# Optimization experiments

Hardware: AMD Instinct MI355X
Metric: run time of the kernel (lower is better)

## Reference

```python
import jax, jax.numpy as jnp
import numpy as np

N_SRC = 50000
N_TGT = 50000
E = 320000
D = 256          # feature dim == hidden_channels
H = 256
OUT = 16
L = 2
P_DROP = 0.1
NEG_SLOPE = 0.01  # F.leaky_relu default


def _seg_mean(x, src_idx, dst_idx, n_dst):
    # gather source features along edges, mean-aggregate per destination (PyG SAGE default aggr='mean')
    msgs = x[src_idx]                                            # [E, D]
    s = jax.ops.segment_sum(msgs, dst_idx, num_segments=n_dst)   # [n_dst, D]
    cnt = jax.ops.segment_sum(jnp.ones((dst_idx.shape[0],), x.dtype), dst_idx, num_segments=n_dst)
    return s / jnp.maximum(cnt, 1.0)[:, None]


def _dropout(x, p, key):
    keep = jax.random.bernoulli(key, 1.0 - p, x.shape)
    return jnp.where(keep, x / (1.0 - p), jnp.zeros((), x.dtype))


def setup_inputs() -> dict:
    key = jax.random.key(0)
    ks = jax.random.split(key, 16)
    sc_in = 1.0 / np.sqrt(D)
    sc_h = 1.0 / np.sqrt(H)
    inp = {
        'x_source': jax.random.normal(ks[0], (N_SRC, D), jnp.float32),
        'x_target': jax.random.normal(ks[1], (N_TGT, D), jnp.float32),
        'ei_st': jax.random.randint(ks[2], (2, E), 0, N_SRC, jnp.int32),  # row0: source idx, row1: target idx
        'ei_ts': jax.random.randint(ks[3], (2, E), 0, N_TGT, jnp.int32),  # row0: target idx, row1: source idx
        # SAGEConv params per layer per relation; lin_l has bias, lin_r does not (PyG)
        'Wl_st': jax.random.normal(ks[4], (L, D, H), jnp.float32) * sc_in,
        'Wr_st': jax.random.normal(ks[5], (L, D, H), jnp.float32) * sc_in,
        'b_st': jnp.zeros((L, H), jnp.float32),
        'Wl_ts': jax.random.normal(ks[6], (L, D, H), jnp.float32) * sc_in,
        'Wr_ts': jax.random.normal(ks[7], (L, D, H), jnp.float32) * sc_in,
        'b_ts': jnp.zeros((L, H), jnp.float32),
        'Wout': jax.random.normal(ks[8], (H, OUT), jnp.float32) * sc_h,
        'bout': jnp.zeros((OUT,), jnp.float32),
    }
    return inp


def reference(x_source, x_target, ei_st, ei_ts, Wl_st, Wr_st, b_st, Wl_ts, Wr_ts, b_ts, Wout, bout):
    drop_key = jax.random.key(42)
    x_s, x_t = x_source, x_target
    for l in range(L):
        # relation ('source','edge','target'): messages source -> target
        m_t = _seg_mean(x_s, ei_st[0], ei_st[1], N_TGT)
        new_t = m_t @ Wl_st[l] + b_st[l] + x_t @ Wr_st[l]
        # relation ('target','rev_edge','source'): messages target -> source
        m_s = _seg_mean(x_t, ei_ts[0], ei_ts[1], N_SRC)
        new_s = m_s @ Wl_ts[l] + b_ts[l] + x_s @ Wr_ts[l]
        # leaky_relu + dropout (F.dropout default training=True)
        new_s = jnp.where(new_s >= 0, new_s, NEG_SLOPE * new_s)
        new_t = jnp.where(new_t >= 0, new_t, NEG_SLOPE * new_t)
        x_s = _dropout(new_s, P_DROP, jax.random.fold_in(drop_key, 2 * l))
        x_t = _dropout(new_t, P_DROP, jax.random.fold_in(drop_key, 2 * l + 1))
    return x_s @ Wout + bout  # [N_SRC, OUT]
```

## Files before the change

### kernel.cpp

```cpp
#include <hip/hip_runtime.h>
#include <stdint.h>

#define NSRC 50000
#define NTGT 50000
#define NE   320000
#define DIN  256
#define HID  256
#define DOUT 16

#define GBM 64
#define GBLK ((NSRC + GBM - 1) / GBM)
#define MASK_DW_PER (GBLK * 512)
#define MASK_BLKS (3 * MASK_DW_PER / 256)

typedef __attribute__((ext_vector_type(8))) short bf16x8;
typedef __attribute__((ext_vector_type(4))) float f32x4;

__device__ inline ushort f2b(float f) {
  uint32_t u = __float_as_uint(f);
  return (ushort)((u + 0x7FFFu + ((u >> 16) & 1u)) >> 16);
}
__device__ inline float b2f(ushort h) { return __uint_as_float(((uint32_t)h) << 16); }

typedef __attribute__((address_space(3))) uint32_t lds_u32_t;
typedef const __attribute__((address_space(1))) uint32_t glb_u32_t;
__device__ __forceinline__ void ld_lds16(const ushort* g, ushort* lds) {
  __builtin_amdgcn_global_load_lds((glb_u32_t*)g, (lds_u32_t*)lds, 16, 0, 0);
}

__host__ __device__ constexpr uint64_t tf2x32(uint32_t k0, uint32_t k1,
                                              uint32_t x0, uint32_t x1) {
  uint32_t ks2 = k0 ^ k1 ^ 0x1BD11BDAu;
  x0 += k0; x1 += k1;
#define TF_ROT(x, r) (((x) << (r)) | ((x) >> (32 - (r))))
#define TF_RND(r) { x0 += x1; x1 = TF_ROT(x1, r) ^ x0; }
  TF_RND(13) TF_RND(15) TF_RND(26) TF_RND(6)
  x0 += k1;  x1 += ks2 + 1u;
  TF_RND(17) TF_RND(29) TF_RND(16) TF_RND(24)
  x0 += ks2; x1 += k0 + 2u;
  TF_RND(13) TF_RND(15) TF_RND(26) TF_RND(6)
  x0 += k0;  x1 += k1 + 3u;
  TF_RND(17) TF_RND(29) TF_RND(16) TF_RND(24)
  x0 += k1;  x1 += ks2 + 4u;
  TF_RND(13) TF_RND(15) TF_RND(26) TF_RND(6)
  x0 += ks2; x1 += k0 + 5u;
#undef TF_RND
#undef TF_ROT
  return (uint64_t(x0) << 32) | uint64_t(x1);
}

constexpr uint64_t FOLD[4] = {
  tf2x32(0u, 42u, 0u, 0u),
  tf2x32(0u, 42u, 0u, 1u),
  tf2x32(0u, 42u, 0u, 2u),
  tf2x32(0u, 42u, 0u, 3u),
};

__global__ __launch_bounds__(256) void cvt2_f32_bf16(const float* __restrict__ a,
                                                     const float* __restrict__ b,
                                                     ushort* __restrict__ oa,
                                                     ushort* __restrict__ ob,
                                                     int n4, int nbPer) {
  int blk = blockIdx.x;
  const float* in = blk < nbPer ? a : b;
  ushort* out = blk < nbPer ? oa : ob;
  int i = (blk % nbPer) * 256 + threadIdx.x;
  if (i >= n4) return;
  float4 v = ((const float4*)in)[i];
  ushort4 o;
  o.x = f2b(v.x); o.y = f2b(v.y); o.z = f2b(v.z); o.w = f2b(v.w);
  ((ushort4*)out)[i] = o;
}

__device__ __forceinline__ void mask_word(uint32_t* __restrict__ masks, int d) {
  int g = d / MASK_DW_PER;
  int w = d - g * MASK_DW_PER;
  int gt = w >> 1, half = w & 1;
  int gblk = gt >> 8, gtid = gt & 255;
  int wave = gtid >> 6, lane = gtid & 63;
  int q = lane >> 4, r = lane & 15;
  uint64_t fk = (g == 0) ? FOLD[1] : (g == 1 ? FOLD[0] : FOLD[2]);
  uint32_t kk0 = (uint32_t)(fk >> 32), kk1 = (uint32_t)fk;
  int mbase = gblk * GBM;
  uint32_t mword = 0;
#pragma unroll
  for (int bb = 0; bb < 32; ++bb) {
    int s = half * 32 + bb;
    int si = s >> 4, se = (s >> 2) & 3, sj = s & 3;
    uint32_t rowg = (uint32_t)(mbase + si * 16 + q * 4 + se);
    uint32_t colg = (uint32_t)(wave * 64 + sj * 16 + r);
    uint64_t rr = tf2x32(kk0, kk1, 0u, rowg * 256u + colg);
    uint32_t bits = (uint32_t)(rr >> 32) ^ (uint32_t)rr;
    mword |= (((bits >> 9) < 7549747u) ? 1u : 0u) << bb;
  }
  masks[d] = mword;
}

struct W6 {
  const float* s[6];
  ushort* d[6];
};
__global__ __launch_bounds__(256) void wcvt_t6(W6 p) {
  __shared__ ushort tile[64][65];
  int w = blockIdx.x >> 4;
  const float* W = p.s[w];
  ushort* Wt = p.d[w];
  int t = threadIdx.x;
  int ktile = (blockIdx.x >> 2) & 3, ntile = blockIdx.x & 3;
#pragma unroll
  for (int rep = 0; rep < 16; ++rep) {
    int lin = rep * 256 + t;
    int kk = lin >> 6, nn = lin & 63;
    tile[nn][kk] = f2b(W[(size_t)(ktile * 64 + kk) * 256 + ntile * 64 + nn]);
  }
  __syncthreads();
#pragma unroll
  for (int rep = 0; rep < 16; ++rep) {
    int lin = rep * 256 + t;
    int nn = lin >> 6, kk = lin & 63;
    Wt[(size_t)(ntile * 64 + nn) * 256 + ktile * 64 + kk] = tile[nn][kk];
  }
}

__global__ __launch_bounds__(256) void csr_hist2(const int* __restrict__ ei_a,
                                                 const int* __restrict__ ei_b,
                                                 int* __restrict__ cur_a,
                                                 int* __restrict__ cur_b,
                                                 int nE, int nbPer) {
  int blk = blockIdx.x;
  const int* ei = blk < nbPer ? ei_a : ei_b;
  int* cur = blk < nbPer ? cur_a : cur_b;
  int e = (blk % nbPer) * 256 + threadIdx.x;
  if (e < nE) atomicAdd(cur + ei[nE + e], 1);
}

#define SB 1024
__global__ __launch_bounds__(SB) void scan_partial(const int* __restrict__ cur_a,
                                                   const int* __restrict__ cur_b,
                                                   int* __restrict__ bsum,
                                                   int n, int nbPer) {
  __shared__ int red[SB];
  int b = blockIdx.x;
  const int* cnt = b < nbPer ? cur_a : cur_b;
  int i = (b % nbPer) * SB + threadIdx.x;
  red[threadIdx.x] = (i < n) ? cnt[i] : 0;
  __syncthreads();
  for (int d = SB / 2; d > 0; d >>= 1) {
    if (threadIdx.x < d) red[threadIdx.x] += red[threadIdx.x + d];
    __syncthreads();
  }
  if (threadIdx.x == 0) bsum[b] = red[0];
}

__global__ __launch_bounds__(128) void scan_base(int* __restrict__ bsum, int nbPer) {
  __shared__ int buf[2][64];
  int half = threadIdx.x >> 6;
  int t = threadIdx.x & 63;
  buf[half][t] = (t < nbPer) ? bsum[half * nbPer + t] : 0;
  __syncthreads();
  for (int d = 1; d < 64; d <<= 1) {
    int v = (t >= d) ? buf[half][t - d] : 0;
    __syncthreads();
    buf[half][t] += v;
    __syncthreads();
  }
  if (t < nbPer) bsum[half * nbPer + t] = (t == 0) ? 0 : buf[half][t - 1];
}

__global__ __launch_bounds__(SB) void scan_final(int* __restrict__ cur_a,
                                                 int* __restrict__ cur_b,
                                                 int* __restrict__ offs_a,
                                                 int* __restrict__ offs_b,
                                                 const int* __restrict__ bsum,
                                                 int n, int nbPer) {
  __shared__ int part[SB];
  int b = blockIdx.x;
  bool first = b < nbPer;
  int* cur = first ? cur_a : cur_b;
  int* offs = first ? offs_a : offs_b;
  int i = (b % nbPer) * SB + threadIdx.x;
  int v = (i < n) ? cur[i] : 0;
  part[threadIdx.x] = v;
  __syncthreads();
  for (int d = 1; d < SB; d <<= 1) {
    int tv = (threadIdx.x >= d) ? part[threadIdx.x - d] : 0;
    __syncthreads();
    part[threadIdx.x] += tv;
    __syncthreads();
  }
  int excl = part[threadIdx.x] - v + bsum[b];
  if (i < n) {
    offs[i] = excl;
    cur[i] = 0;
  }
  if (i == n - 1) offs[n] = excl + v;
}

__global__ __launch_bounds__(256) void csr_fill2(const int* __restrict__ ei_a,
                                                 const int* __restrict__ ei_b,
                                                 const int* __restrict__ offs_a,
                                                 const int* __restrict__ offs_b,
                                                 int* __restrict__ cur_a,
                                                 int* __restrict__ cur_b,
                                                 int* __restrict__ adj_a,
                                                 int* __restrict__ adj_b,
                                                 int nE, int nbPer) {
  int blk = blockIdx.x;
  bool first = blk < nbPer;
  const int* ei = first ? ei_a : ei_b;
  const int* offs = first ? offs_a : offs_b;
  int* cur = first ? cur_a : cur_b;
  int* adj = first ? adj_a : adj_b;
  int e = (blk % nbPer) * 256 + threadIdx.x;
  if (e >= nE) return;
  int dst = ei[nE + e];
  int pos = atomicAdd(cur + dst, 1);
  adj[offs[dst] + pos] = ei[e];
}

__device__ __forceinline__ void gather_row(const ushort* __restrict__ x,
                                           const int* __restrict__ offs,
                                           const int* __restrict__ adj,
                                           ushort* __restrict__ m,
                                           int row, int lane) {
  int start = offs[row], end = offs[row + 1];
  float a0 = 0.f, a1 = 0.f, a2 = 0.f, a3 = 0.f;
  int e = start;
  for (; e + 3 < end; e += 4) {
    int s0 = adj[e], s1 = adj[e + 1], s2 = adj[e + 2], s3 = adj[e + 3];
    ushort4 v0 = *(const ushort4*)(x + (size_t)s0 * DIN + lane * 4);
    ushort4 v1 = *(const ushort4*)(x + (size_t)s1 * DIN + lane * 4);
    ushort4 v2 = *(const ushort4*)(x + (size_t)s2 * DIN + lane * 4);
    ushort4 v3 = *(const ushort4*)(x + (size_t)s3 * DIN + lane * 4);
    a0 += b2f(v0.x); a1 += b2f(v0.y); a2 += b2f(v0.z); a3 += b2f(v0.w);
    a0 += b2f(v1.x); a1 += b2f(v1.y); a2 += b2f(v1.z); a3 += b2f(v1.w);
    a0 += b2f(v2.x); a1 += b2f(v2.y); a2 += b2f(v2.z); a3 += b2f(v2.w);
    a0 += b2f(v3.x); a1 += b2f(v3.y); a2 += b2f(v3.z); a3 += b2f(v3.w);
  }
  for (; e < end; ++e) {
    int s = adj[e];
    ushort4 v = *(const ushort4*)(x + (size_t)s * DIN + lane * 4);
    a0 += b2f(v.x); a1 += b2f(v.y); a2 += b2f(v.z); a3 += b2f(v.w);
  }
  float inv = 1.0f / fmaxf((float)(end - start), 1.0f);
  ushort4 o;
  o.x = f2b(a0 * inv); o.y = f2b(a1 * inv); o.z = f2b(a2 * inv); o.w = f2b(a3 * inv);
  *(ushort4*)(m + (size_t)row * DIN + lane * 4) = o;
}

__global__ __launch_bounds__(256) void gather_mean_h(const ushort* __restrict__ x,
                                                     const int* __restrict__ offs,
                                                     const int* __restrict__ adj,
                                                     ushort* __restrict__ m,
                                                     int nRows) {
  int row = blockIdx.x * 4 + (threadIdx.x >> 6);
  if (row >= nRows) return;
  gather_row(x, offs, adj, m, row, threadIdx.x & 63);
}

__global__ __launch_bounds__(256) void gather2m_mean_h(
    const ushort* __restrict__ xa, const int* __restrict__ offsa,
    const int* __restrict__ adja, ushort* __restrict__ ma,
    const ushort* __restrict__ xb, const int* __restrict__ offsb,
    const int* __restrict__ adjb, ushort* __restrict__ mb,
    uint32_t* __restrict__ masks, int nRows, int nbPer) {
  const int T = 2 * nbPer + MASK_BLKS;
  int blk = (int)(((long long)blockIdx.x * 97) % T);
  if (blk >= 2 * nbPer) {
    mask_word(masks, (blk - 2 * nbPer) * 256 + threadIdx.x);
    return;
  }
  bool first = blk < nbPer;
  int row = (blk % nbPer) * 4 + (threadIdx.x >> 6);
  if (row >= nRows) return;
  if (first) gather_row(xa, offsa, adja, ma, row, threadIdx.x & 63);
  else       gather_row(xb, offsb, adjb, mb, row, threadIdx.x & 63);
}

__global__ __launch_bounds__(256, 4) void gemm_dual_mfma(
    const ushort* __restrict__ A1, const ushort* __restrict__ A2,
    const ushort* __restrict__ W1t, const ushort* __restrict__ W2t,
    const float* __restrict__ bias, const uint2* __restrict__ mk,
    ushort* __restrict__ C, int M) {
  __shared__ ushort sA[2][GBM * 32];
  __shared__ ushort sB[2][HID * 32];
  const int tid = threadIdx.x;
  const int wave = tid >> 6, lane = tid & 63;
  const int q = lane >> 4, r = lane & 15;
  const int mbase = blockIdx.x * GBM;

  const uint2 km = mk[blockIdx.x * 256 + tid];

  f32x4 acc[4][4] = {};

  const int arow = tid >> 2;
  const int akc = (tid & 3) * 8;
  const int agrow = min(mbase + arow, M - 1);
  const ushort* a1p = A1 + (size_t)agrow * DIN + akc;
  const ushort* a2p = A2 + (size_t)agrow * DIN + akc;
  const ushort* w1b = W1t + (size_t)arow * DIN + akc;
  const ushort* w2b = W2t + (size_t)arow * DIN + akc;
  ushort* ldsA0 = &sA[0][wave * 512];
  ushort* ldsA1 = &sA[1][wave * 512];

#pragma unroll
  for (int t = 0; t < 8; ++t) {
    const int kt = t * 32;
    __syncthreads();
    ld_lds16(a1p + kt, ldsA0);
    ld_lds16(a2p + kt, ldsA1);
#pragma unroll
    for (int c = 0; c < 4; ++c) {
      ld_lds16(w1b + c * (64 * DIN) + kt, &sB[0][c * 2048 + wave * 512]);
      ld_lds16(w2b + c * (64 * DIN) + kt, &sB[1][c * 2048 + wave * 512]);
    }
    __syncthreads();
#pragma unroll
    for (int ph = 0; ph < 2; ++ph) {
      bf16x8 af[4], bfr[4];
#pragma unroll
      for (int i = 0; i < 4; ++i)
        af[i] = *(const bf16x8*)&sA[ph][(i * 16 + r) * 32 + q * 8];
#pragma unroll
      for (int j = 0; j < 4; ++j)
        bfr[j] = *(const bf16x8*)&sB[ph][(wave * 64 + j * 16 + r) * 32 + q * 8];
#pragma unroll
      for (int i = 0; i < 4; ++i)
#pragma unroll
        for (int j = 0; j < 4; ++j)
          acc[i][j] = __builtin_amdgcn_mfma_f32_16x16x32_bf16(af[i], bfr[j],
                                                              acc[i][j], 0, 0, 0);
    }
  }

  float bj[4];
#pragma unroll
  for (int j = 0; j < 4; ++j) bj[j] = bias[wave * 64 + j * 16 + r];
#pragma unroll
  for (int i = 0; i < 4; ++i) {
#pragma unroll
    for (int e = 0; e < 4; ++e) {
      int rowg = mbase + i * 16 + q * 4 + e;
      if (rowg >= M) continue;
#pragma unroll
      for (int j = 0; j < 4; ++j) {
        const int s = i * 16 + e * 4 + j;
        int colg = wave * 64 + j * 16 + r;
        float v = acc[i][j][e] + bj[j];
        v = v >= 0.0f ? v : 0.01f * v;
        uint32_t keep = ((s < 32 ? km.x >> s : km.y >> (s - 32)) & 1u);
        v = keep ? v * (1.0f / 0.9f) : 0.0f;
        C[(size_t)rowg * HID + colg] = f2b(v);
      }
    }
  }
}

__global__ __launch_bounds__(256) void out_gemm_h(const ushort* __restrict__ X,
                                                  const float* __restrict__ Wout,
                                                  const float* __restrict__ bout,
                                                  float* __restrict__ C, int M) {
  __shared__ float sW[DIN * DOUT];
  int tid = threadIdx.x;
#pragma unroll
  for (int i = 0; i < (DIN * DOUT) / 256; ++i) sW[i * 256 + tid] = Wout[i * 256 + tid];
  __syncthreads();
  int rr = tid >> 4, c = tid & 15;
  int row = blockIdx.x * 16 + rr;
  if (row >= M) return;
  float acc = bout[c];
  const ushort* xp = X + (size_t)row * DIN;
  for (int k = 0; k < DIN; k += 8) {
    uint4 u = *(const uint4*)(xp + k);
    const ushort* us = (const ushort*)&u;
#pragma unroll
    for (int t = 0; t < 8; ++t) acc += b2f(us[t]) * sW[(k + t) * DOUT + c];
  }
  C[(size_t)row * DOUT + c] = acc;
}

extern "C" void kernel_launch(void* const* d_in, const int* in_sizes, int n_in,
                              void* d_out, int out_size, void* d_ws, size_t ws_size,
                              hipStream_t stream) {
  const float* x_source = (const float*)d_in[0];
  const float* x_target = (const float*)d_in[1];
  const int* ei_st = (const int*)d_in[2];
  const int* ei_ts = (const int*)d_in[3];
  const float* Wl_st = (const float*)d_in[4];
  const float* Wr_st = (const float*)d_in[5];
  const float* b_st  = (const float*)d_in[6];
  const float* Wl_ts = (const float*)d_in[7];
  const float* Wr_ts = (const float*)d_in[8];
  const float* b_ts  = (const float*)d_in[9];
  const float* Wout  = (const float*)d_in[10];
  const float* bout  = (const float*)d_in[11];
  float* out = (float*)d_out;

  const size_t F = (size_t)NSRC * DIN;
  const size_t WM = (size_t)DIN * HID;
  const int nbScan = (NSRC + SB - 1) / SB;
  const size_t intCount = (NTGT + 1) + (NSRC + 1) + 2 * NE + NTGT + NSRC +
                          2 * nbScan + 3 * MASK_DW_PER;
  const size_t need = (5 * F + 6 * WM) * sizeof(ushort) + intCount * sizeof(int);
  if (ws_size < need) return;

  ushort* xs0h = (ushort*)d_ws;
  ushort* xt0h = xs0h + F;
  ushort* B0h  = xt0h + F;
  ushort* B1h  = B0h + F;
  ushort* B2h  = B1h + F;
  ushort* wt0  = B2h + F;
  ushort* wt1  = wt0 + WM;
  ushort* wt2  = wt1 + WM;
  ushort* wt3  = wt2 + WM;
  ushort* wt4  = wt3 + WM;
  ushort* wt5  = wt4 + WM;
  int* ip      = (int*)(wt5 + WM);
  int* offs_st = ip;
  int* offs_ts = offs_st + NTGT + 1;
  int* adj_st  = offs_ts + NSRC + 1;
  int* adj_ts  = adj_st + NE;
  int* cur_t   = adj_ts + NE;
  int* cur_s   = cur_t + NTGT;
  int* bsum    = cur_s + NSRC;
  uint32_t* masks = (uint32_t*)(bsum + 2 * nbScan);

  const int EB = (NE + 255) / 256;
  const int CB = (int)(F / 4 + 255) / 256;
  const int GGB = (int)((NTGT / 4));

  cvt2_f32_bf16<<<2 * CB, 256, 0, stream>>>(x_source, x_target, xs0h, xt0h,
                                            (int)(F / 4), CB);
  W6 wb;
  wb.s[0] = Wl_st;      wb.d[0] = wt0;
  wb.s[1] = Wr_st;      wb.d[1] = wt1;
  wb.s[2] = Wl_ts;      wb.d[2] = wt2;
  wb.s[3] = Wr_ts;      wb.d[3] = wt3;
  wb.s[4] = Wl_ts + WM; wb.d[4] = wt4;
  wb.s[5] = Wr_ts + WM; wb.d[5] = wt5;
  wcvt_t6<<<96, 256, 0, stream>>>(wb);

  hipMemsetAsync(cur_t, 0, (NTGT + NSRC) * sizeof(int), stream);
  csr_hist2<<<2 * EB, 256, 0, stream>>>(ei_st, ei_ts, cur_t, cur_s, NE, EB);
  scan_partial<<<2 * nbScan, SB, 0, stream>>>(cur_t, cur_s, bsum, NTGT, nbScan);
  scan_base<<<1, 128, 0, stream>>>(bsum, nbScan);
  scan_final<<<2 * nbScan, SB, 0, stream>>>(cur_t, cur_s, offs_st, offs_ts,
                                            bsum, NTGT, nbScan);
  csr_fill2<<<2 * EB, 256, 0, stream>>>(ei_st, ei_ts, offs_st, offs_ts,
                                        cur_t, cur_s, adj_st, adj_ts, NE, EB);

  gather2m_mean_h<<<2 * GGB + MASK_BLKS, 256, 0, stream>>>(
      xs0h, offs_st, adj_st, B0h, xt0h, offs_ts, adj_ts, B1h, masks, NTGT, GGB);

  gemm_dual_mfma<<<GBLK, 256, 0, stream>>>(
      B0h, xt0h, wt0, wt1, b_st, (const uint2*)(masks), B2h, NTGT);
  gemm_dual_mfma<<<GBLK, 256, 0, stream>>>(
      B1h, xs0h, wt2, wt3, b_ts, (const uint2*)(masks + MASK_DW_PER), B0h, NSRC);

  gather_mean_h<<<GGB, 256, 0, stream>>>(B2h, offs_ts, adj_ts, B1h, NSRC);
  gemm_dual_mfma<<<GBLK, 256, 0, stream>>>(
      B1h, B0h, wt4, wt5, b_ts + HID, (const uint2*)(masks + 2 * MASK_DW_PER),
      B2h, NSRC);

  out_gemm_h<<<(NSRC + 15) / 16, 256, 0, stream>>>(B2h, Wout, bout, out, NSRC);
}
```

Measured before the change: 466.1 us.

## Merge prep kernels into one launch and overlap layer-2 gather with GEMM

Folds the input bf16 conversion, weight transpose-conversion, CSR histogram and dropout-mask generation into a single interleaved prep kernel, and co-schedules the second-layer gather with the second first-layer GEMM in one launch. The gather result is written into the now-free xt0h buffer, which the final GEMM reads. The aim is fewer launches and kernel-boundary bubbles, with independent work filling the idle slots. The gemm_gather launch keeps the GEMM's LDS footprint for the gather blocks, which could reduce their occupancy.

```diff
diff --git a/kernel.cpp b/kernel.cpp
--- a/kernel.cpp
+++ b/kernel.cpp
@@ -56,22 +56,6 @@
   tf2x32(0u, 42u, 0u, 3u),
 };
 
-__global__ __launch_bounds__(256) void cvt2_f32_bf16(const float* __restrict__ a,
-                                                     const float* __restrict__ b,
-                                                     ushort* __restrict__ oa,
-                                                     ushort* __restrict__ ob,
-                                                     int n4, int nbPer) {
-  int blk = blockIdx.x;
-  const float* in = blk < nbPer ? a : b;
-  ushort* out = blk < nbPer ? oa : ob;
-  int i = (blk % nbPer) * 256 + threadIdx.x;
-  if (i >= n4) return;
-  float4 v = ((const float4*)in)[i];
-  ushort4 o;
-  o.x = f2b(v.x); o.y = f2b(v.y); o.z = f2b(v.z); o.w = f2b(v.w);
-  ((ushort4*)out)[i] = o;
-}
-
 __device__ __forceinline__ void mask_word(uint32_t* __restrict__ masks, int d) {
   int g = d / MASK_DW_PER;
   int w = d - g * MASK_DW_PER;
@@ -96,42 +80,65 @@
   masks[d] = mword;
 }
 
-struct W6 {
-  const float* s[6];
-  ushort* d[6];
+#define NB_CVT  25000
+#define NB_W    96
+#define NB_HIST 2500
+#define PREP_T  (NB_CVT + NB_W + NB_HIST + MASK_BLKS)
+
+struct PrepArgs {
+  const float *xs, *xt;
+  ushort *oxs, *oxt;
+  const float* wsrc[6];
+  ushort* wdst[6];
+  const int *ei_a, *ei_b;
+  int *cur_a, *cur_b;
+  uint32_t* masks;
 };
-__global__ __launch_bounds__(256) void wcvt_t6(W6 p) {
+
+__global__ __launch_bounds__(256) void prep_kernel(PrepArgs p) {
   __shared__ ushort tile[64][65];
-  int w = blockIdx.x >> 4;
-  const float* W = p.s[w];
-  ushort* Wt = p.d[w];
-  int t = threadIdx.x;
-  int ktile = (blockIdx.x >> 2) & 3, ntile = blockIdx.x & 3;
-#pragma unroll
-  for (int rep = 0; rep < 16; ++rep) {
-    int lin = rep * 256 + t;
-    int kk = lin >> 6, nn = lin & 63;
-    tile[nn][kk] = f2b(W[(size_t)(ktile * 64 + kk) * 256 + ntile * 64 + nn]);
-  }
-  __syncthreads();
-#pragma unroll
-  for (int rep = 0; rep < 16; ++rep) {
-    int lin = rep * 256 + t;
-    int nn = lin >> 6, kk = lin & 63;
-    Wt[(size_t)(ntile * 64 + nn) * 256 + ktile * 64 + kk] = tile[nn][kk];
-  }
-}
-
-__global__ __launch_bounds__(256) void csr_hist2(const int* __restrict__ ei_a,
-                                                 const int* __restrict__ ei_b,
-                                                 int* __restrict__ cur_a,
-                                                 int* __restrict__ cur_b,
-                                                 int nE, int nbPer) {
-  int blk = blockIdx.x;
-  const int* ei = blk < nbPer ? ei_a : ei_b;
-  int* cur = blk < nbPer ? cur_a : cur_b;
-  int e = (blk % nbPer) * 256 + threadIdx.x;
-  if (e < nE) atomicAdd(cur + ei[nE + e], 1);
+  int blk = (int)(((long long)blockIdx.x * 97) % PREP_T);
+  int tid = threadIdx.x;
+  if (blk < NB_CVT) {
+    const float* in = blk < (NB_CVT / 2) ? p.xs : p.xt;
+    ushort* out = blk < (NB_CVT / 2) ? p.oxs : p.oxt;
+    int i = (blk % (NB_CVT / 2)) * 256 + tid;
+    float4 v = ((const float4*)in)[i];
+    ushort4 o;
+    o.x = f2b(v.x); o.y = f2b(v.y); o.z = f2b(v.z); o.w = f2b(v.w);
+    ((ushort4*)out)[i] = o;
+    return;
+  }
+  blk -= NB_CVT;
+  if (blk < NB_W) {
+    const float* W = p.wsrc[blk >> 4];
+    ushort* Wt = p.wdst[blk >> 4];
+    int ktile = (blk >> 2) & 3, ntile = blk & 3;
+#pragma unroll
+    for (int rep = 0; rep < 16; ++rep) {
+      int lin = rep * 256 + tid;
+      int kk = lin >> 6, nn = lin & 63;
+      tile[nn][kk] = f2b(W[(size_t)(ktile * 64 + kk) * 256 + ntile * 64 + nn]);
+    }
+    __syncthreads();
+#pragma unroll
+    for (int rep = 0; rep < 16; ++rep) {
+      int lin = rep * 256 + tid;
+      int nn = lin >> 6, kk = lin & 63;
+      Wt[(size_t)(ntile * 64 + nn) * 256 + ktile * 64 + kk] = tile[nn][kk];
+    }
+    return;
+  }
+  blk -= NB_W;
+  if (blk < NB_HIST) {
+    const int* ei = blk < (NB_HIST / 2) ? p.ei_a : p.ei_b;
+    int* cur = blk < (NB_HIST / 2) ? p.cur_a : p.cur_b;
+    int e = (blk % (NB_HIST / 2)) * 256 + tid;
+    if (e < NE) atomicAdd(cur + ei[NE + e], 1);
+    return;
+  }
+  blk -= NB_HIST;
+  mask_word(p.masks, blk * 256 + tid);
 }
 
 #define SB 1024
@@ -248,28 +255,13 @@
   *(ushort4*)(m + (size_t)row * DIN + lane * 4) = o;
 }
 
-__global__ __launch_bounds__(256) void gather_mean_h(const ushort* __restrict__ x,
-                                                     const int* __restrict__ offs,
-                                                     const int* __restrict__ adj,
-                                                     ushort* __restrict__ m,
-                                                     int nRows) {
-  int row = blockIdx.x * 4 + (threadIdx.x >> 6);
-  if (row >= nRows) return;
-  gather_row(x, offs, adj, m, row, threadIdx.x & 63);
-}
-
-__global__ __launch_bounds__(256) void gather2m_mean_h(
+__global__ __launch_bounds__(256) void gather2_mean_h(
     const ushort* __restrict__ xa, const int* __restrict__ offsa,
     const int* __restrict__ adja, ushort* __restrict__ ma,
     const ushort* __restrict__ xb, const int* __restrict__ offsb,
     const int* __restrict__ adjb, ushort* __restrict__ mb,
-    uint32_t* __restrict__ masks, int nRows, int nbPer) {
-  const int T = 2 * nbPer + MASK_BLKS;
-  int blk = (int)(((long long)blockIdx.x * 97) % T);
-  if (blk >= 2 * nbPer) {
-    mask_word(masks, (blk - 2 * nbPer) * 256 + threadIdx.x);
-    return;
-  }
+    int nRows, int nbPer) {
+  int blk = blockIdx.x;
   bool first = blk < nbPer;
   int row = (blk % nbPer) * 4 + (threadIdx.x >> 6);
   if (row >= nRows) return;
@@ -277,19 +269,17 @@
   else       gather_row(xb, offsb, adjb, mb, row, threadIdx.x & 63);
 }
 
-__global__ __launch_bounds__(256, 4) void gemm_dual_mfma(
-    const ushort* __restrict__ A1, const ushort* __restrict__ A2,
+__device__ __forceinline__ void gemm_body(
+    int bid, const ushort* __restrict__ A1, const ushort* __restrict__ A2,
     const ushort* __restrict__ W1t, const ushort* __restrict__ W2t,
     const float* __restrict__ bias, const uint2* __restrict__ mk,
-    ushort* __restrict__ C, int M) {
-  __shared__ ushort sA[2][GBM * 32];
-  __shared__ ushort sB[2][HID * 32];
+    ushort* __restrict__ C, int M, ushort* sA, ushort* sB) {
   const int tid = threadIdx.x;
   const int wave = tid >> 6, lane = tid & 63;
   const int q = lane >> 4, r = lane & 15;
-  const int mbase = blockIdx.x * GBM;
-
-  const uint2 km = mk[blockIdx.x * 256 + tid];
+  const int mbase = bid * GBM;
+
+  const uint2 km = mk[bid * 256 + tid];
 
   f32x4 acc[4][4] = {};
 
@@ -300,8 +290,8 @@
   const ushort* a2p = A2 + (size_t)agrow * DIN + akc;
   const ushort* w1b = W1t + (size_t)arow * DIN + akc;
   const ushort* w2b = W2t + (size_t)arow * DIN + akc;
-  ushort* ldsA0 = &sA[0][wave * 512];
-  ushort* ldsA1 = &sA[1][wave * 512];
+  ushort* ldsA0 = sA + wave * 512;
+  ushort* ldsA1 = sA + 2048 + wave * 512;
 
 #pragma unroll
   for (int t = 0; t < 8; ++t) {
@@ -311,8 +301,8 @@
     ld_lds16(a2p + kt, ldsA1);
 #pragma unroll
     for (int c = 0; c < 4; ++c) {
-      ld_lds16(w1b + c * (64 * DIN) + kt, &sB[0][c * 2048 + wave * 512]);
-      ld_lds16(w2b + c * (64 * DIN) + kt, &sB[1][c * 2048 + wave * 512]);
+      ld_lds16(w1b + c * (64 * DIN) + kt, sB + c * 2048 + wave * 512);
+      ld_lds16(w2b + c * (64 * DIN) + kt, sB + 8192 + c * 2048 + wave * 512);
     }
     __syncthreads();
 #pragma unroll
@@ -320,10 +310,10 @@
       bf16x8 af[4], bfr[4];
 #pragma unroll
       for (int i = 0; i < 4; ++i)
-        af[i] = *(const bf16x8*)&sA[ph][(i * 16 + r) * 32 + q * 8];
+        af[i] = *(const bf16x8*)&sA[ph * 2048 + (i * 16 + r) * 32 + q * 8];
 #pragma unroll
       for (int j = 0; j < 4; ++j)
-        bfr[j] = *(const bf16x8*)&sB[ph][(wave * 64 + j * 16 + r) * 32 + q * 8];
+        bfr[j] = *(const bf16x8*)&sB[ph * 8192 + (wave * 64 + j * 16 + r) * 32 + q * 8];
 #pragma unroll
       for (int i = 0; i < 4; ++i)
 #pragma unroll
@@ -353,6 +343,37 @@
         C[(size_t)rowg * HID + colg] = f2b(v);
       }
     }
+  }
+}
+
+__global__ __launch_bounds__(256, 4) void gemm_dual_mfma(
+    const ushort* __restrict__ A1, const ushort* __restrict__ A2,
+    const ushort* __restrict__ W1t, const ushort* __restrict__ W2t,
+    const float* __restrict__ bias, const uint2* __restrict__ mk,
+    ushort* __restrict__ C, int M) {
+  __shared__ ushort sA[2][GBM * 32];
+  __shared__ ushort sB[2][HID * 32];
+  gemm_body(blockIdx.x, A1, A2, W1t, W2t, bias, mk, C, M, &sA[0][0], &sB[0][0]);
+}
+
+#define GG_GB 12500
+#define GG_T  (GBLK + GG_GB)
+
+__global__ __launch_bounds__(256, 4) void gemm_gather(
+    const ushort* __restrict__ A1, const ushort* __restrict__ A2,
+    const ushort* __restrict__ W1t, const ushort* __restrict__ W2t,
+    const float* __restrict__ bias, const uint2* __restrict__ mk,
+    ushort* __restrict__ C, int M,
+    const ushort* __restrict__ gx, const int* __restrict__ goffs,
+    const int* __restrict__ gadj, ushort* __restrict__ gm, int gRows) {
+  __shared__ ushort sA[2][GBM * 32];
+  __shared__ ushort sB[2][HID * 32];
+  int blk = (int)(((long long)blockIdx.x * 101) % GG_T);
+  if (blk < GBLK) {
+    gemm_body(blk, A1, A2, W1t, W2t, bias, mk, C, M, &sA[0][0], &sB[0][0]);
+  } else {
+    int row = (blk - GBLK) * 4 + (threadIdx.x >> 6);
+    if (row < gRows) gather_row(gx, goffs, gadj, gm, row, threadIdx.x & 63);
   }
 }
 
@@ -426,22 +447,22 @@
   uint32_t* masks = (uint32_t*)(bsum + 2 * nbScan);
 
   const int EB = (NE + 255) / 256;
-  const int CB = (int)(F / 4 + 255) / 256;
-  const int GGB = (int)((NTGT / 4));
-
-  cvt2_f32_bf16<<<2 * CB, 256, 0, stream>>>(x_source, x_target, xs0h, xt0h,
-                                            (int)(F / 4), CB);
-  W6 wb;
-  wb.s[0] = Wl_st;      wb.d[0] = wt0;
-  wb.s[1] = Wr_st;      wb.d[1] = wt1;
-  wb.s[2] = Wl_ts;      wb.d[2] = wt2;
-  wb.s[3] = Wr_ts;      wb.d[3] = wt3;
-  wb.s[4] = Wl_ts + WM; wb.d[4] = wt4;
-  wb.s[5] = Wr_ts + WM; wb.d[5] = wt5;
-  wcvt_t6<<<96, 256, 0, stream>>>(wb);
+  const int GGB = NTGT / 4;
 
   hipMemsetAsync(cur_t, 0, (NTGT + NSRC) * sizeof(int), stream);
-  csr_hist2<<<2 * EB, 256, 0, stream>>>(ei_st, ei_ts, cur_t, cur_s, NE, EB);
+  PrepArgs pa;
+  pa.xs = x_source; pa.xt = x_target; pa.oxs = xs0h; pa.oxt = xt0h;
+  pa.wsrc[0] = Wl_st;      pa.wdst[0] = wt0;
+  pa.wsrc[1] = Wr_st;      pa.wdst[1] = wt1;
+  pa.wsrc[2] = Wl_ts;      pa.wdst[2] = wt2;
+  pa.wsrc[3] = Wr_ts;      pa.wdst[3] = wt3;
+  pa.wsrc[4] = Wl_ts + WM; pa.wdst[4] = wt4;
+  pa.wsrc[5] = Wr_ts + WM; pa.wdst[5] = wt5;
+  pa.ei_a = ei_st; pa.ei_b = ei_ts;
+  pa.cur_a = cur_t; pa.cur_b = cur_s;
+  pa.masks = masks;
+  prep_kernel<<<PREP_T, 256, 0, stream>>>(pa);
+
   scan_partial<<<2 * nbScan, SB, 0, stream>>>(cur_t, cur_s, bsum, NTGT, nbScan);
   scan_base<<<1, 128, 0, stream>>>(bsum, nbScan);
   scan_final<<<2 * nbScan, SB, 0, stream>>>(cur_t, cur_s, offs_st, offs_ts,
@@ -449,17 +470,19 @@
   csr_fill2<<<2 * EB, 256, 0, stream>>>(ei_st, ei_ts, offs_st, offs_ts,
                                         cur_t, cur_s, adj_st, adj_ts, NE, EB);
 
-  gather2m_mean_h<<<2 * GGB + MASK_BLKS, 256, 0, stream>>>(
-      xs0h, offs_st, adj_st, B0h, xt0h, offs_ts, adj_ts, B1h, masks, NTGT, GGB);
+  gather2_mean_h<<<2 * GGB, 256, 0, stream>>>(xs0h, offs_st, adj_st, B0h,
+                                              xt0h, offs_ts, adj_ts, B1h,
+                                              NTGT, GGB);
 
   gemm_dual_mfma<<<GBLK, 256, 0, stream>>>(
       B0h, xt0h, wt0, wt1, b_st, (const uint2*)(masks), B2h, NTGT);
+
+  gemm_gather<<<GG_T, 256, 0, stream>>>(
+      B1h, xs0h, wt2, wt3, b_ts, (const uint2*)(masks + MASK_DW_PER), B0h, NSRC,
+      B2h, offs_ts, adj_ts, xt0h, NSRC);
+
   gemm_dual_mfma<<<GBLK, 256, 0, stream>>>(
-      B1h, xs0h, wt2, wt3, b_ts, (const uint2*)(masks + MASK_DW_PER), B0h, NSRC);
-
-  gather_mean_h<<<GGB, 256, 0, stream>>>(B2h, offs_ts, adj_ts, B1h, NSRC);
-  gemm_dual_mfma<<<GBLK, 256, 0, stream>>>(
-      B1h, B0h, wt4, wt5, b_ts + HID, (const uint2*)(masks + 2 * MASK_DW_PER),
+      xt0h, B0h, wt4, wt5, b_ts + HID, (const uint2*)(masks + 2 * MASK_DW_PER),
       B2h, NSRC);
 
   out_gemm_h<<<(NSRC + 15) / 16, 256, 0, stream>>>(B2h, Wout, bout, out, NSRC);
```

Measured after the change: 446.3 us. -4.3%, faster.
